# Kernel optimization log

Hardware: AMD Instinct MI355X
Metric: run time of the kernel (lower is better)

Reference implementation:

```python
import jax, jax.numpy as jnp
import numpy as np

STRIDE = 50
SIZES = (16.0, 32.0, 64.0)
RATIOS = (0.5, 1.0, 2.0)
THRESH = 0.95
IMG_H, IMG_W = 4200, 3200  # input is [N,1,IMG_H,IMG_W]


def _anchors(Hf, Wf):
    # torchvision-style anchors: 3 sizes x 3 aspect ratios = 9 per cell
    r = np.sqrt(np.array(RATIOS, dtype=np.float32))
    s = np.array(SIZES, dtype=np.float32)
    ws = (s[:, None] / r[None, :]).reshape(-1)  # [9]
    hs = (s[:, None] * r[None, :]).reshape(-1)  # [9]
    base = np.stack([-ws / 2, -hs / 2, ws / 2, hs / 2], axis=1)  # [9,4] x1,y1,x2,y2
    sx = (np.arange(Wf, dtype=np.float32) + 0.5) * STRIDE  # [Wf]
    sy = (np.arange(Hf, dtype=np.float32) + 0.5) * STRIDE  # [Hf]
    gx, gy = np.broadcast_arrays(sx[None, :], sy[:, None])  # [Hf,Wf]
    shift = np.stack([gx, gy, gx, gy], axis=-1)  # [Hf,Wf,4]
    return jnp.asarray(shift[:, :, None, :] + base[None, None, :, :])  # [Hf,Wf,9,4]


def _conv(x, w, b, stride, pad):
    y = jax.lax.conv_general_dilated(x, w, window_strides=stride, padding=pad,
                                     dimension_numbers=('NCHW', 'OIHW', 'NCHW'))
    return y + b[None, :, None, None]


def setup_inputs() -> dict:
    key = jax.random.key(0)
    ks = jax.random.split(key, 7)
    return {
        'X': jax.random.normal(ks[0], (8, 1, IMG_H, IMG_W), dtype=jnp.float32),
        'conv_w': jax.random.normal(ks[1], (2, 1, 50, 50), dtype=jnp.float32) * 0.02,
        'conv_b': jax.random.normal(ks[2], (2,), dtype=jnp.float32) * 0.02,
        'box_w': jax.random.normal(ks[3], (36, 2, 3, 3), dtype=jnp.float32) * 0.02,
        'box_b': jax.random.normal(ks[4], (36,), dtype=jnp.float32) * 0.02,
        'cls_w': jax.random.normal(ks[5], (2, 2, 3, 3), dtype=jnp.float32) * 0.5,
        'cls_b': jax.random.normal(ks[6], (2,), dtype=jnp.float32) * 0.5,
    }


def reference(X, conv_w, conv_b, box_w, box_b, cls_w, cls_b):
    feats = _conv(X, conv_w, conv_b, (STRIDE, STRIDE), 'VALID')        # [N,2,84,64]
    N, _, Hf, Wf = feats.shape
    off = _conv(feats, box_w, box_b, (1, 1), 'SAME')                   # [N,36,Hf,Wf]
    off = off.reshape(N, 9, 4, Hf, Wf).transpose(0, 3, 4, 1, 2)        # [N,Hf,Wf,9,4]
    cls = jax.nn.softmax(_conv(feats, cls_w, cls_b, (1, 1), 'SAME'), axis=1)  # Softmax2d
    mask = cls[:, 1] > THRESH                                          # [N,Hf,Wf]
    boxes = _anchors(Hf, Wf)[None] + off                               # offsets applied to anchors
    boxes = jnp.stack([
        jnp.clip(boxes[..., 0], 0.0, float(IMG_W)),
        jnp.clip(boxes[..., 1], 0.0, float(IMG_H)),
        jnp.clip(boxes[..., 2], 0.0, float(IMG_W)),
        jnp.clip(boxes[..., 3], 0.0, float(IMG_H)),
    ], axis=-1)
    # fixed-shape analogue of masked_select: zero out below-threshold anchors
    return boxes * mask[:, :, :, None, None].astype(boxes.dtype)
```

## Files before the change

### kernel.cpp

```cpp
#include <hip/hip_runtime.h>

#define IMG_H 4200
#define IMG_W 3200
#define HF 84
#define WF 64
#define NB 8

__global__ __launch_bounds__(256) void conv1_kernel(
    const float* __restrict__ X, const float* __restrict__ cw,
    const float* __restrict__ cb, float* __restrict__ feats ) {
    __shared__ float4 wlds[1250];
    const int tid = threadIdx.x;
    for (int e = tid; e < 1250; e += 256) {
        wlds[e] = make_float4(cw[2 * e], cw[2 * e + 1], cw[2500 + 2 * e], cw[2500 + 2 * e + 1]);
    }
    __syncthreads();
    const int wave = tid >> 6;
    const int lane = tid & 63;
    const int t = blockIdx.x * 4 + wave;
    const int j = t % WF;
    const int i = (t / WF) % HF;
    const int n = t / (WF * HF);
    const float* base = X + ((size_t)n * IMG_H + (size_t)i * 50) * IMG_W + j * 50;
    float acc0 = 0.f, acc1 = 0.f;
#pragma unroll
    for (int it = 0; it < 20; ++it) {
        int e2 = it * 64 + lane;
        if (e2 < 1250) {
            int ky = e2 / 25;
            int kx = (e2 - ky * 25) * 2;
            const float2 x = *(const float2*)(base + (size_t)ky * IMG_W + kx);
            float4 w = wlds[e2];
            acc0 = fmaf(x.x, w.x, fmaf(x.y, w.y, acc0));
            acc1 = fmaf(x.x, w.z, fmaf(x.y, w.w, acc1));
        }
    }
#pragma unroll
    for (int off = 32; off; off >>= 1) {
        acc0 += __shfl_down(acc0, off, 64);
        acc1 += __shfl_down(acc1, off, 64);
    }
    if (lane == 0) {
        ((float2*)feats)[t] = make_float2(acc0 + cb[0], acc1 + cb[1]);
    }
}

__global__ __launch_bounds__(256) void head_kernel(
    const float* __restrict__ feats, const float* __restrict__ bw,
    const float* __restrict__ bb, const float* __restrict__ clw,
    const float* __restrict__ clb, float* __restrict__ out) {
    __shared__ float s_bw[648];
    __shared__ float s_bb[36];
    __shared__ float s_cw[36];
    __shared__ float s_cb[2];
    const int tid = threadIdx.x;
    for (int e = tid; e < 648; e += 256) s_bw[e] = bw[e];
    if (tid < 36) { s_bb[tid] = bb[tid]; s_cw[tid] = clw[tid]; }
    if (tid < 2) s_cb[tid] = clb[tid];
    __syncthreads();

    const int p = blockIdx.x * 256 + tid;
    const int j = p % WF;
    const int rem = p / WF;
    const int y = rem % HF;
    const int n = rem / HF;

    float f0[3][3], f1[3][3];
#pragma unroll
    for (int dy = 0; dy < 3; ++dy) {
        int yy = y + dy - 1;
#pragma unroll
        for (int dx = 0; dx < 3; ++dx) {
            int xx = j + dx - 1;
            float2 v = make_float2(0.f, 0.f);
            if (yy >= 0 && yy < HF && xx >= 0 && xx < WF)
                v = ((const float2*)feats)[(n * HF + yy) * WF + xx];
            f0[dy][dx] = v.x;
            f1[dy][dx] = v.y;
        }
    }

    float c0 = s_cb[0], c1 = s_cb[1];
#pragma unroll
    for (int ky = 0; ky < 3; ++ky)
#pragma unroll
        for (int kx = 0; kx < 3; ++kx) {
            int k = ky * 3 + kx;
            c0 = fmaf(f0[ky][kx], s_cw[k], c0);
            c0 = fmaf(f1[ky][kx], s_cw[9 + k], c0);
            c1 = fmaf(f0[ky][kx], s_cw[18 + k], c1);
            c1 = fmaf(f1[ky][kx], s_cw[27 + k], c1);
        }
    float mx = fmaxf(c0, c1);
    float e0 = expf(c0 - mx), e1 = expf(c1 - mx);
    float p1 = e1 / (e0 + e1);
    const float maskf = (p1 > 0.95f) ? 1.f : 0.f;

    const float gx = (j + 0.5f) * 50.f;
    const float gy = (y + 0.5f) * 50.f;
    const float wsv[9] = {22.627417f, 16.f, 11.3137085f,
                          45.254834f, 32.f, 22.627417f,
                          90.509668f, 64.f, 45.254834f};
    const float hsv[9] = {11.3137085f, 16.f, 22.627417f,
                          22.627417f, 32.f, 45.254834f,
                          45.254834f, 64.f, 90.509668f};

    float4* outp = (float4*)out + (size_t)p * 9;
#pragma unroll
    for (int a = 0; a < 9; ++a) {
        float o[4];
#pragma unroll
        for (int c = 0; c < 4; ++c) {
            const int ch = a * 4 + c;
            const float* w = &s_bw[ch * 18];
            float acc = s_bb[ch];
#pragma unroll
            for (int ky = 0; ky < 3; ++ky)
#pragma unroll
                for (int kx = 0; kx < 3; ++kx) {
                    int k = ky * 3 + kx;
                    acc = fmaf(f0[ky][kx], w[k], acc);
                    acc = fmaf(f1[ky][kx], w[9 + k], acc);
                }
            o[c] = acc;
        }
        const float hw = 0.5f * wsv[a], hh = 0.5f * hsv[a];
        float x1 = fminf(fmaxf(gx - hw + o[0], 0.f), 3200.f);
        float y1 = fminf(fmaxf(gy - hh + o[1], 0.f), 4200.f);
        float x2 = fminf(fmaxf(gx + hw + o[2], 0.f), 3200.f);
        float y2 = fminf(fmaxf(gy + hh + o[3], 0.f), 4200.f);
        outp[a] = make_float4(x1 * maskf, y1 * maskf, x2 * maskf, y2 * maskf);
    }
}

extern "C" void kernel_launch(void* const* d_in, const int* in_sizes, int n_in,
                              void* d_out, int out_size, void* d_ws, size_t ws_size,
                              hipStream_t stream) {
    const float* X   = (const float*)d_in[0];
    const float* cw  = (const float*)d_in[1];
    const float* cb  = (const float*)d_in[2];
    const float* bw  = (const float*)d_in[3];
    const float* bb  = (const float*)d_in[4];
    const float* clw = (const float*)d_in[5];
    const float* clb = (const float*)d_in[6];
    float* out = (float*)d_out;
    float* feats = (float*)d_ws;

    conv1_kernel<<<10752, 256, 0, stream>>>(X, cw, cb, feats);
    head_kernel<<<168, 256, 0, stream>>>(feats, bw, bb, clw, clb, out);
}
```

Before: 562.4 us.

## Stream conv1 input rows into LDS with double-buffered global_load_lds per output row

The strided 50x50 conv is restructured so that each block computes one full output row of 64 columns instead of each wave computing a single output. The block streams the 50 contiguous input rows into a double-buffered LDS row buffer with async global-to-LDS loads, and each lane handles one output column. The four waves split the kernel-x range between them and combine their partial sums through LDS at the end. The goal is fully coalesced, contiguous reads of the 430MB input instead of scattered float2 patch loads, plus overlap of the next row's load with compute. The trade-off is far fewer blocks (672), a barrier per row, and a larger LDS footprint, which may limit latency hiding.

```diff
diff --git a/kernel.cpp b/kernel.cpp
--- a/kernel.cpp
+++ b/kernel.cpp
@@ -6,42 +6,80 @@
 #define WF 64
 #define NB 8
 
+typedef const __attribute__((address_space(1))) unsigned int* gl_p;
+typedef __attribute__((address_space(3))) unsigned int* lds_p;
+
+__device__ __forceinline__ void gl_lds16(const void* g, void* l) {
+    __builtin_amdgcn_global_load_lds((gl_p)g, (lds_p)l, 16, 0, 0);
+}
+
 __global__ __launch_bounds__(256) void conv1_kernel(
     const float* __restrict__ X, const float* __restrict__ cw,
     const float* __restrict__ cb, float* __restrict__ feats ) {
-    __shared__ float4 wlds[1250];
+    __shared__ float2 w2[2500];
+    __shared__ __align__(16) float4 rowbuf[2][800];
+    __shared__ float2 part[3][WF];
+
     const int tid = threadIdx.x;
-    for (int e = tid; e < 1250; e += 256) {
-        wlds[e] = make_float4(cw[2 * e], cw[2 * e + 1], cw[2500 + 2 * e], cw[2500 + 2 * e + 1]);
+    const int wave = tid >> 6;
+    const int lane = tid & 63;
+    const int b = blockIdx.x;
+    const int n = b / HF;
+    const int i = b - n * HF;
+
+    for (int e = tid; e < 2500; e += 256)
+        w2[e] = make_float2(cw[e], cw[2500 + e]);
+
+    const float* Xrow0 = X + ((size_t)n * IMG_H + (size_t)i * 50) * IMG_W;
+
+    {
+        const float4* s = (const float4*)Xrow0;
+        gl_lds16(s + tid,       &rowbuf[0][tid]);
+        gl_lds16(s + tid + 256, &rowbuf[0][tid + 256]);
+        gl_lds16(s + tid + 512, &rowbuf[0][tid + 512]);
+        if (tid < 32) gl_lds16(s + tid + 768, &rowbuf[0][tid + 768]);
     }
     __syncthreads();
-    const int wave = tid >> 6;
-    const int lane = tid & 63;
-    const int t = blockIdx.x * 4 + wave;
-    const int j = t % WF;
-    const int i = (t / WF) % HF;
-    const int n = t / (WF * HF);
-    const float* base = X + ((size_t)n * IMG_H + (size_t)i * 50) * IMG_W + j * 50;
+
+    const int kx0 = wave * 12 + (wave < 2 ? wave : 2);
+    const int len = (wave < 2) ? 13 : 12;
     float acc0 = 0.f, acc1 = 0.f;
+
+    for (int ky = 0; ky < 50; ++ky) {
+        const int cur = ky & 1;
+        if (ky < 49) {
+            const float4* s = (const float4*)(Xrow0 + (size_t)(ky + 1) * IMG_W);
+            float4* d = rowbuf[cur ^ 1];
+            gl_lds16(s + tid,       d + tid);
+            gl_lds16(s + tid + 256, d + tid + 256);
+            gl_lds16(s + tid + 512, d + tid + 512);
+            if (tid < 32) gl_lds16(s + tid + 768, d + tid + 768);
+        }
+        const float* rowf = (const float*)rowbuf[cur];
+        const float2* wrow = &w2[ky * 50];
 #pragma unroll
-    for (int it = 0; it < 20; ++it) {
-        int e2 = it * 64 + lane;
-        if (e2 < 1250) {
-            int ky = e2 / 25;
-            int kx = (e2 - ky * 25) * 2;
-            const float2 x = *(const float2*)(base + (size_t)ky * IMG_W + kx);
-            float4 w = wlds[e2];
-            acc0 = fmaf(x.x, w.x, fmaf(x.y, w.y, acc0));
-            acc1 = fmaf(x.x, w.z, fmaf(x.y, w.w, acc1));
+        for (int t = 0; t < 13; ++t) {
+            if (t < len) {
+                const int kx = kx0 + t;
+                const float xv = rowf[lane * 50 + kx];
+                const float2 w = wrow[kx];
+                acc0 = fmaf(xv, w.x, acc0);
+                acc1 = fmaf(xv, w.y, acc1);
+            }
         }
+        __syncthreads();
     }
+
+    if (wave > 0) part[wave - 1][lane] = make_float2(acc0, acc1);
+    __syncthreads();
+    if (wave == 0) {
 #pragma unroll
-    for (int off = 32; off; off >>= 1) {
-        acc0 += __shfl_down(acc0, off, 64);
-        acc1 += __shfl_down(acc1, off, 64);
-    }
-    if (lane == 0) {
-        ((float2*)feats)[t] = make_float2(acc0 + cb[0], acc1 + cb[1]);
+        for (int w = 0; w < 3; ++w) {
+            acc0 += part[w][lane].x;
+            acc1 += part[w][lane].y;
+        }
+        ((float2*)feats)[(n * HF + i) * WF + lane] =
+            make_float2(acc0 + cb[0], acc1 + cb[1]);
     }
 }
 
@@ -146,6 +184,6 @@
     float* out = (float*)d_out;
     float* feats = (float*)d_ws;
 
-    conv1_kernel<<<10752, 256, 0, stream>>>(X, cw, cb, feats);
+    conv1_kernel<<<672, 256, 0, stream>>>(X, cw, cb, feats);
     head_kernel<<<168, 256, 0, stream>>>(feats, bw, bb, clw, clb, out);
 }
```

Result: slower. 576.9 us (+2.6%).
